# Kernel optimization log

Hardware: AMD Instinct MI355X
Metric: run time of the kernel (lower is better)

## Reference

```python
import jax, jax.numpy as jnp
import numpy as np

VOCAB, EMBED, HIDDEN, LAYERS = 32000, 1024, 1024, 2
BATCH, SEQ = 128, 256


def setup_inputs() -> dict:
    key = jax.random.key(0)
    ks = jax.random.split(key, 6)
    source = jax.random.randint(ks[0], (BATCH, SEQ), 0, VOCAB)
    emb_W = jax.random.normal(ks[1], (VOCAB, EMBED), dtype=jnp.float32) * 0.01
    s = 1.0 / np.sqrt(HIDDEN)
    W_ih = jax.random.uniform(ks[2], (LAYERS, 3 * HIDDEN, EMBED), jnp.float32, -s, s)
    W_hh = jax.random.uniform(ks[3], (LAYERS, 3 * HIDDEN, HIDDEN), jnp.float32, -s, s)
    b_ih = jax.random.uniform(ks[4], (LAYERS, 3 * HIDDEN), jnp.float32, -s, s)
    b_hh = jax.random.uniform(ks[5], (LAYERS, 3 * HIDDEN), jnp.float32, -s, s)
    return {"source": source, "emb_W": emb_W, "W_ih": W_ih, "W_hh": W_hh,
            "b_ih": b_ih, "b_hh": b_hh}


def _gru_layer(xs, h0, Wih, Whh, bih, bhh):
    # xs: [S, B, in], h0: [B, H]; PyTorch GRU cell math.
    def step(h, x):
        gi = x @ Wih.T + bih          # [B, 3H]
        gh = h @ Whh.T + bhh          # [B, 3H]
        ir, iz, inn = jnp.split(gi, 3, axis=-1)
        hr, hz, hn = jnp.split(gh, 3, axis=-1)
        r = jax.nn.sigmoid(ir + hr)
        z = jax.nn.sigmoid(iz + hz)
        n = jnp.tanh(inn + r * hn)
        h_new = (1.0 - z) * n + z * h
        return h_new, h_new
    hT, ys = jax.lax.scan(step, h0, xs)
    return ys, hT


def reference(source, emb_W, W_ih, W_hh, b_ih, b_hh):
    # embedding with transpose=True: [S, B, E]
    embed = emb_W[source.T]
    B = source.shape[0]
    x = embed
    finals = []
    for l in range(W_ih.shape[0]):
        h0 = jnp.zeros((B, W_hh.shape[-1]), dtype=embed.dtype)
        x, hT = _gru_layer(x, h0, W_ih[l], W_hh[l], b_ih[l], b_hh[l])
        finals.append(hT)
    state = jnp.stack(finals, axis=0)  # [L, B, H]
    return x, state
```

## Files before the change

kernel.cpp:

```cpp
#include <hip/hip_runtime.h>
#include <cstdint>
#include <cstddef>

#define SEQ 256
#define BATCH 128
#define HID 1024
#define H3 3072
#define TCH 32
#define NCH (SEQ/TCH)
#define CROWS (TCH*BATCH)

typedef __bf16 bf16x8 __attribute__((ext_vector_type(8)));
typedef float f32x4 __attribute__((ext_vector_type(4)));
typedef unsigned short ushort8 __attribute__((ext_vector_type(8)));
typedef unsigned long long u64x2 __attribute__((ext_vector_type(2)));

static __device__ __forceinline__ unsigned short f2bf(float f){
  unsigned int u = __float_as_uint(f);
  u += 0x7fffu + ((u >> 16) & 1u);
  return (unsigned short)(u >> 16);
}
static __device__ __forceinline__ float sigm(float x){
  return 1.0f / (1.0f + __expf(-x));
}
static __device__ __forceinline__ float tanh_(float x){
  x = fminf(15.0f, fmaxf(-15.0f, x));
  float e = __expf(2.0f * x);
  return (e - 1.0f) / (e + 1.0f);
}


__global__ __launch_bounds__(256) void cvt_bf16(const float* __restrict__ in,
                                                unsigned short* __restrict__ out, int n4){
  int i = blockIdx.x * blockDim.x + threadIdx.x;
  int stride = gridDim.x * blockDim.x;
  for (; i < n4; i += stride){
    float4 v = reinterpret_cast<const float4*>(in)[i];
    ushort4 o = { f2bf(v.x), f2bf(v.y), f2bf(v.z), f2bf(v.w) };
    reinterpret_cast<ushort4*>(out)[i] = o;
  }
}

__global__ __launch_bounds__(256) void embed_gather(const int* __restrict__ src,
                                                    const float* __restrict__ embW,
                                                    unsigned short* __restrict__ x0){
  int bx = blockIdx.x;
  int s = bx >> 7, b = bx & 127;
  int row = src[b * SEQ + s];
  float4 v = reinterpret_cast<const float4*>(embW + (size_t)row * HID)[threadIdx.x];
  ushort4 o = { f2bf(v.x), f2bf(v.y), f2bf(v.z), f2bf(v.w) };
  reinterpret_cast<ushort4*>(x0 + (size_t)bx * HID)[threadIdx.x] = o;
}

__global__ __launch_bounds__(256) void zero_u32(unsigned* __restrict__ p, int n){
  int i = blockIdx.x * blockDim.x + threadIdx.x;
  if (i < n) p[i] = 0u;
}

#define BM 128
#define BN 128
#define BK 32
#define LDT 40

__global__ __launch_bounds__(256) void gemm_xw(
    const unsigned short* __restrict__ A,
    const unsigned short* __restrict__ B,
    float* __restrict__ C)
{
  __shared__ unsigned short As[2][BM][LDT];
  __shared__ unsigned short Bs[2][BN][LDT];
  int tid = threadIdx.x;
  int lane = tid & 63, wid = tid >> 6;
  int fr = lane & 15, kg = lane >> 4;
  int wr = wid >> 1, wc = wid & 1;
  int brow = blockIdx.x * BM;
  int bcol = blockIdx.y * BN;

  int r0 = tid >> 2;
  int r1 = 64 + (tid >> 2);
  int k8 = (tid & 3) * 8;

  const unsigned short* Ab = A + (size_t)brow * HID;
  const unsigned short* Bb = B + (size_t)bcol * HID;

  f32x4 acc[4][4] = {};
  ushort8 a0, a1, b0, b1;

  a0 = *(const ushort8*)(Ab + (size_t)r0 * HID + k8);
  a1 = *(const ushort8*)(Ab + (size_t)r1 * HID + k8);
  b0 = *(const ushort8*)(Bb + (size_t)r0 * HID + k8);
  b1 = *(const ushort8*)(Bb + (size_t)r1 * HID + k8);
  *(ushort8*)&As[0][r0][k8] = a0;
  *(ushort8*)&As[0][r1][k8] = a1;
  *(ushort8*)&Bs[0][r0][k8] = b0;
  *(ushort8*)&Bs[0][r1][k8] = b1;
  __syncthreads();

  for (int kt = 0; kt < HID / BK; ++kt){
    int cur = kt & 1;
    if (kt < HID / BK - 1){
      int ko = (kt + 1) * BK + k8;
      a0 = *(const ushort8*)(Ab + (size_t)r0 * HID + ko);
      a1 = *(const ushort8*)(Ab + (size_t)r1 * HID + ko);
      b0 = *(const ushort8*)(Bb + (size_t)r0 * HID + ko);
      b1 = *(const ushort8*)(Bb + (size_t)r1 * HID + ko);
    }
    bf16x8 af[4], bfr[4];
    #pragma unroll
    for (int m = 0; m < 4; ++m)
      af[m] = *(const bf16x8*)&As[cur][wr*64 + m*16 + fr][kg*8];
    #pragma unroll
    for (int n = 0; n < 4; ++n)
      bfr[n] = *(const bf16x8*)&Bs[cur][wc*64 + n*16 + fr][kg*8];
    #pragma unroll
    for (int m = 0; m < 4; ++m)
      #pragma unroll
      for (int n = 0; n < 4; ++n)
        acc[m][n] = __builtin_amdgcn_mfma_f32_16x16x32_bf16(af[m], bfr[n], acc[m][n], 0,0,0);
    if (kt < HID / BK - 1){
      int nxt = cur ^ 1;
      *(ushort8*)&As[nxt][r0][k8] = a0;
      *(ushort8*)&As[nxt][r1][k8] = a1;
      *(ushort8*)&Bs[nxt][r0][k8] = b0;
      *(ushort8*)&Bs[nxt][r1][k8] = b1;
      __syncthreads();
    }
  }

  #pragma unroll
  for (int m = 0; m < 4; ++m){
    int rowb = brow + wr*64 + m*16 + kg*4;
    #pragma unroll
    for (int n = 0; n < 4; ++n){
      int col = bcol + wc*64 + n*16 + fr;
      *(f32x4*)(C + (size_t)col * CROWS + rowb) = acc[m][n];
    }
  }
}

#define LDW 1032

__global__ __launch_bounds__(256) void gru_persist(
    const unsigned short* __restrict__ Whh,
    const float* __restrict__ bih,
    const float* __restrict__ bhh,
    const float* __restrict__ gi,
    float* __restrict__ ys_out,
    unsigned short* __restrict__ x_next,
    unsigned long long* __restrict__ hbA,
    unsigned long long* __restrict__ hbB,
    float* __restrict__ hf32,
    float* __restrict__ state_out,
    int t0,
    unsigned* __restrict__ cnt)
{
  __shared__ unsigned short Wlds[48 * LDW];
  __shared__ f32x4 red[4][2][3][64];
  __shared__ unsigned short hvt[32][16];

  int tid = threadIdx.x;
  int lane = tid & 63, wid = tid >> 6;
  int ct = blockIdx.x & 63, rg = blockIdx.x >> 6;
  int c0 = ct * 16, rowbase = rg * 32;
  int fr = lane & 15, kg = lane >> 4;

  #pragma unroll
  for (int j = 0; j < 24; ++j){
    int cid = j * 256 + tid;
    int r = cid >> 7, k8 = (cid & 127) * 8;
    int grow = (r >> 4) * HID + c0 + (r & 15);
    *(ushort8*)&Wlds[r * LDW + k8] = *(const ushort8*)(Whh + (size_t)grow * HID + k8);
  }

  int crow = tid >> 3;
  int ccol = (tid << 1) & 15;
  int rt_ = crow >> 4, r16 = crow & 15, kq = r16 >> 2, qq = r16 & 3;
  int l0 = kq * 16 + ccol, l1 = l0 + 1;
  int colc0 = c0 + ccol, colc1 = colc0 + 1;
  int growL = rowbase + crow;

  float br0 = bih[colc0] + bhh[colc0];
  float bz0 = bih[HID + colc0] + bhh[HID + colc0];
  float bi0 = bih[2*HID + colc0];
  float bh0 = bhh[2*HID + colc0];
  float br1 = bih[colc1] + bhh[colc1];
  float bz1 = bih[HID + colc1] + bhh[HID + colc1];
  float bi1 = bih[2*HID + colc1];
  float bh1 = bhh[2*HID + colc1];

  float hprev0 = 0.0f, hprev1 = 0.0f;
  if (t0 > 0){
    hprev0 = hf32[(size_t)growL * HID + colc0];
    hprev1 = hf32[(size_t)growL * HID + colc1];
  }
  __syncthreads();

  for (int s = 0; s < TCH; ++s){
    int t = t0 + s;
    size_t gro = (size_t)s * BATCH + growL;
    float gr0 = gi[(size_t)(0*HID + colc0) * CROWS + gro];
    float gz0 = gi[(size_t)(1*HID + colc0) * CROWS + gro];
    float gn0 = gi[(size_t)(2*HID + colc0) * CROWS + gro];
    float gr1 = gi[(size_t)(0*HID + colc1) * CROWS + gro];
    float gz1 = gi[(size_t)(1*HID + colc1) * CROWS + gro];
    float gn1 = gi[(size_t)(2*HID + colc1) * CROWS + gro];

    if (s > 0){
      if (tid == 0){
        unsigned* p = cnt + rg * TCH + (s - 1);
        int lim = 4000000;
        while (__hip_atomic_load(p, __ATOMIC_RELAXED, __HIP_MEMORY_SCOPE_AGENT) < 64u
               && --lim)
          __builtin_amdgcn_s_sleep(1);
      }
      __syncthreads();
      asm volatile("" ::: "memory");
    }
    const unsigned long long* hin = (t & 1) ? hbB : hbA;
    unsigned long long*       hout = (t & 1) ? hbA : hbB;

    f32x4 acc[2][3] = {};
    if (t > 0){
      const int wk0 = wid << 8;
      bf16x8 a[2][8];
      #pragma unroll
      for (int rt = 0; rt < 2; ++rt){
        size_t rb = (size_t)(rowbase + rt*16 + fr) * HID + wk0 + kg*8;
        #pragma unroll
        for (int j = 0; j < 8; ++j){
          size_t ui = (rb + (size_t)j*32) >> 2;
          unsigned long long u0 = __hip_atomic_load(hin + ui,     __ATOMIC_RELAXED, __HIP_MEMORY_SCOPE_AGENT);
          unsigned long long u1 = __hip_atomic_load(hin + ui + 1, __ATOMIC_RELAXED, __HIP_MEMORY_SCOPE_AGENT);
          u64x2 uu; uu[0] = u0; uu[1] = u1;
          a[rt][j] = __builtin_bit_cast(bf16x8, uu);
        }
      }
      #pragma unroll
      for (int j = 0; j < 8; ++j){
        int bo = wk0 + j*32 + kg*8;
        bf16x8 b0 = *(const bf16x8*)&Wlds[(     fr) * LDW + bo];
        bf16x8 b1 = *(const bf16x8*)&Wlds[(16 + fr) * LDW + bo];
        bf16x8 b2 = *(const bf16x8*)&Wlds[(32 + fr) * LDW + bo];
        acc[0][0] = __builtin_amdgcn_mfma_f32_16x16x32_bf16(a[0][j], b0, acc[0][0], 0,0,0);
        acc[0][1] = __builtin_amdgcn_mfma_f32_16x16x32_bf16(a[0][j], b1, acc[0][1], 0,0,0);
        acc[0][2] = __builtin_amdgcn_mfma_f32_16x16x32_bf16(a[0][j], b2, acc[0][2], 0,0,0);
        acc[1][0] = __builtin_amdgcn_mfma_f32_16x16x32_bf16(a[1][j], b0, acc[1][0], 0,0,0);
        acc[1][1] = __builtin_amdgcn_mfma_f32_16x16x32_bf16(a[1][j], b1, acc[1][1], 0,0,0);
        acc[1][2] = __builtin_amdgcn_mfma_f32_16x16x32_bf16(a[1][j], b2, acc[1][2], 0,0,0);
      }
    }

    #pragma unroll
    for (int rt = 0; rt < 2; ++rt)
      #pragma unroll
      for (int g = 0; g < 3; ++g)
        red[wid][rt][g][lane] = acc[rt][g];
    __syncthreads();

    float v0[3], v1[3];
    #pragma unroll
    for (int g = 0; g < 3; ++g){
      float s0 = 0.f, s1 = 0.f;
      #pragma unroll
      for (int w = 0; w < 4; ++w){
        s0 += red[w][rt_][g][l0][qq];
        s1 += red[w][rt_][g][l1][qq];
      }
      v0[g] = s0; v1[g] = s1;
    }

    float rA = sigm(gr0 + v0[0] + br0);
    float zA = sigm(gz0 + v0[1] + bz0);
    float nA = tanh_(gn0 + bi0 + rA * (v0[2] + bh0));
    float h0 = (1.0f - zA) * nA + zA * hprev0;
    float rB = sigm(gr1 + v1[0] + br1);
    float zB = sigm(gz1 + v1[1] + bz1);
    float nB = tanh_(gn1 + bi1 + rB * (v1[2] + bh1));
    float h1 = (1.0f - zB) * nB + zB * hprev1;
    hprev0 = h0; hprev1 = h1;

    if (ys_out){
      float2 yv = { h0, h1 };
      *(float2*)&ys_out[((size_t)t * BATCH + growL) * HID + colc0] = yv;
    }
    if (x_next){
      ushort2 xv = { f2bf(h0), f2bf(h1) };
      *(ushort2*)&x_next[((size_t)s * BATCH + growL) * HID + colc0] = xv;
    }
    if (t == SEQ-1){
      float2 sv = { h0, h1 };
      *(float2*)&state_out[(size_t)growL * HID + colc0] = sv;
    }
    if (s == TCH-1){
      float2 hv2 = { h0, h1 };
      *(float2*)&hf32[(size_t)growL * HID + colc0] = hv2;
    }

    ushort2 hb2 = { f2bf(h0), f2bf(h1) };
    *(ushort2*)&hvt[crow][ccol] = hb2;
    __syncthreads();

    if (tid < 128){
      int row = tid >> 2, c4 = (tid & 3) * 4;
      unsigned long long u = *(const unsigned long long*)&hvt[row][c4];
      __hip_atomic_store(hout + (((size_t)(rowbase + row) * HID + c0 + c4) >> 2), u,
                         __ATOMIC_RELAXED, __HIP_MEMORY_SCOPE_AGENT);
    }
    __syncthreads();

    if (tid == 0 && s < TCH-1)
      __hip_atomic_fetch_add(cnt + rg * TCH + s, 1u,
                             __ATOMIC_RELAXED, __HIP_MEMORY_SCOPE_AGENT);
  }
}


extern "C" void kernel_launch(void* const* d_in, const int* in_sizes, int n_in,
                              void* d_out, int out_size, void* d_ws, size_t ws_size,
                              hipStream_t stream){
  (void)in_sizes; (void)n_in; (void)out_size; (void)ws_size;
  const int*   src  = (const int*)  d_in[0];
  const float* embW = (const float*)d_in[1];
  const float* Wih  = (const float*)d_in[2];
  const float* Whh  = (const float*)d_in[3];
  const float* bih  = (const float*)d_in[4];
  const float* bhh  = (const float*)d_in[5];
  float* out = (float*)d_out;

  char* ws = (char*)d_ws;
  size_t off = 0;
  auto carve = [&](size_t bytes) -> void* {
    void* p = ws + off;
    off += (bytes + 255) & ~(size_t)255;
    return p;
  };
  const size_t WELEM = (size_t)2 * H3 * HID;
  unsigned short* wihb = (unsigned short*)carve(WELEM * 2);
  unsigned short* whhb = (unsigned short*)carve(WELEM * 2);
  unsigned short* x0   = (unsigned short*)carve((size_t)SEQ*BATCH*HID*2);
  unsigned short* x1   = (unsigned short*)carve((size_t)SEQ*BATCH*HID*2);
  float*          gi   = (float*)         carve((size_t)CROWS*H3*4);
  unsigned long long* hbA = (unsigned long long*)carve((size_t)BATCH*HID*2);
  unsigned long long* hbB = (unsigned long long*)carve((size_t)BATCH*HID*2);
  float*          hf32 = (float*)         carve((size_t)BATCH*HID*4);
  unsigned*       cnt  = (unsigned*)      carve((size_t)16 * 4 * TCH * 4);

  cvt_bf16<<<2048, 256, 0, stream>>>(Wih, wihb, (int)(WELEM/4));
  cvt_bf16<<<2048, 256, 0, stream>>>(Whh, whhb, (int)(WELEM/4));
  embed_gather<<<SEQ*BATCH, 256, 0, stream>>>(src, embW, x0);
  zero_u32<<<8, 256, 0, stream>>>(cnt, 16 * 4 * TCH);

  float* state = out + (size_t)SEQ*BATCH*HID;
  for (int l = 0; l < 2; ++l){
    const float* bihl = bih + l*H3;
    const float* bhhl = bhh + l*H3;
    const unsigned short* wl = wihb + (size_t)l*H3*HID;
    const unsigned short* vl = whhb + (size_t)l*H3*HID;
    for (int cch = 0; cch < NCH; ++cch){
      const unsigned short* Achunk = (l == 0) ? (x0 + (size_t)cch*CROWS*HID)
                                              : (x1 + (size_t)cch*CROWS*HID);
      gemm_xw<<<dim3(CROWS/BM, H3/BN), 256, 0, stream>>>(Achunk, wl, gi);
      int launch_id = l*NCH + cch;
      gru_persist<<<256, 256, 0, stream>>>(
          vl, bihl, bhhl, gi,
          (l == 1) ? out : nullptr,
          (l == 0) ? (x1 + (size_t)cch*CROWS*HID) : nullptr,
          hbA, hbB, hf32,
          state + (size_t)l*BATCH*HID,
          cch*TCH,
          cnt + (size_t)launch_id * 4 * TCH);
    }
  }
}
```

Before: 3.769 ms.

## Restructure GRU recurrence into per-wave row slices with flag-array dependency sync

The persistent GRU kernel now runs 128 threads per block, and each wave owns a 16-row batch slice and computes the full K=1024 reduction itself. This removes the cross-wave LDS reduction and most block-level barriers. The single counter per row group with one polling thread is replaced by per-(step, row slice, column tile) flags, which every lane of a wave polls together. Each wave therefore waits only for the 64 producers of its own 16 rows. The gi inputs for the next step are prefetched and the final hidden state is stored in a lane-native layout. In exchange, each wave does a longer serial MFMA chain, the workspace needs a much larger flag array, and memory ordering now relies on manual waitcnt fences.

```diff
diff --git a/kernel.cpp b/kernel.cpp
--- a/kernel.cpp
+++ b/kernel.cpp
@@ -140,7 +140,7 @@
 
 #define LDW 1032
 
-__global__ __launch_bounds__(256) void gru_persist(
+__global__ __launch_bounds__(128) void gru_persist(
     const unsigned short* __restrict__ Whh,
     const float* __restrict__ bih,
     const float* __restrict__ bhh,
@@ -152,165 +152,135 @@
     float* __restrict__ hf32,
     float* __restrict__ state_out,
     int t0,
-    unsigned* __restrict__ cnt)
+    unsigned* __restrict__ flags)
 {
   __shared__ unsigned short Wlds[48 * LDW];
-  __shared__ f32x4 red[4][2][3][64];
-  __shared__ unsigned short hvt[32][16];
+  __shared__ unsigned short hvt[2][16][16];
 
   int tid = threadIdx.x;
-  int lane = tid & 63, wid = tid >> 6;
-  int ct = blockIdx.x & 63, rg = blockIdx.x >> 6;
-  int c0 = ct * 16, rowbase = rg * 32;
+  int lane = tid & 63, w = tid >> 6;
+  int ct = blockIdx.x & 63, rgp = blockIdx.x >> 6;
+  int c0 = ct * 16;
+  int rs = rgp * 2 + w;
+  int R0 = rs * 16;
   int fr = lane & 15, kg = lane >> 4;
 
   #pragma unroll
-  for (int j = 0; j < 24; ++j){
-    int cid = j * 256 + tid;
+  for (int j = 0; j < 48; ++j){
+    int cid = j * 128 + tid;
     int r = cid >> 7, k8 = (cid & 127) * 8;
     int grow = (r >> 4) * HID + c0 + (r & 15);
     *(ushort8*)&Wlds[r * LDW + k8] = *(const ushort8*)(Whh + (size_t)grow * HID + k8);
   }
 
-  int crow = tid >> 3;
-  int ccol = (tid << 1) & 15;
-  int rt_ = crow >> 4, r16 = crow & 15, kq = r16 >> 2, qq = r16 & 3;
-  int l0 = kq * 16 + ccol, l1 = l0 + 1;
-  int colc0 = c0 + ccol, colc1 = colc0 + 1;
-  int growL = rowbase + crow;
-
-  float br0 = bih[colc0] + bhh[colc0];
-  float bz0 = bih[HID + colc0] + bhh[HID + colc0];
-  float bi0 = bih[2*HID + colc0];
-  float bh0 = bhh[2*HID + colc0];
-  float br1 = bih[colc1] + bhh[colc1];
-  float bz1 = bih[HID + colc1] + bhh[HID + colc1];
-  float bi1 = bih[2*HID + colc1];
-  float bh1 = bhh[2*HID + colc1];
-
-  float hprev0 = 0.0f, hprev1 = 0.0f;
-  if (t0 > 0){
-    hprev0 = hf32[(size_t)growL * HID + colc0];
-    hprev1 = hf32[(size_t)growL * HID + colc1];
-  }
+  int col = c0 + fr;
+  float br_ = bih[col] + bhh[col];
+  float bz_ = bih[HID + col] + bhh[HID + col];
+  float bi_ = bih[2*HID + col];
+  float bh_ = bhh[2*HID + col];
+
+  float* hf_lane = hf32 + (((size_t)blockIdx.x * 2 + w) * 64 + lane) * 4;
+  f32x4 hprev = {0,0,0,0};
+  if (t0 > 0) hprev = *(const f32x4*)hf_lane;
+
+  const float* gib = gi + (size_t)col * CROWS + R0 + kg * 4;
+  const size_t GOFF = (size_t)HID * CROWS;
+
   __syncthreads();
+
+  f32x4 g_r = *(const f32x4*)(gib);
+  f32x4 g_z = *(const f32x4*)(gib + GOFF);
+  f32x4 g_n = *(const f32x4*)(gib + 2*GOFF);
 
   for (int s = 0; s < TCH; ++s){
     int t = t0 + s;
-    size_t gro = (size_t)s * BATCH + growL;
-    float gr0 = gi[(size_t)(0*HID + colc0) * CROWS + gro];
-    float gz0 = gi[(size_t)(1*HID + colc0) * CROWS + gro];
-    float gn0 = gi[(size_t)(2*HID + colc0) * CROWS + gro];
-    float gr1 = gi[(size_t)(0*HID + colc1) * CROWS + gro];
-    float gz1 = gi[(size_t)(1*HID + colc1) * CROWS + gro];
-    float gn1 = gi[(size_t)(2*HID + colc1) * CROWS + gro];
 
     if (s > 0){
-      if (tid == 0){
-        unsigned* p = cnt + rg * TCH + (s - 1);
-        int lim = 4000000;
-        while (__hip_atomic_load(p, __ATOMIC_RELAXED, __HIP_MEMORY_SCOPE_AGENT) < 64u
-               && --lim)
-          __builtin_amdgcn_s_sleep(1);
+      const unsigned* fp = flags + ((s - 1) * 8 + rs) * 64;
+      int lim = 2000000;
+      for (;;){
+        unsigned f = __hip_atomic_load(fp + lane, __ATOMIC_RELAXED, __HIP_MEMORY_SCOPE_AGENT);
+        if (__all(f != 0) || !--lim) break;
+        __builtin_amdgcn_s_sleep(1);
       }
-      __syncthreads();
-      asm volatile("" ::: "memory");
-    }
-    const unsigned long long* hin = (t & 1) ? hbB : hbA;
-    unsigned long long*       hout = (t & 1) ? hbA : hbB;
-
-    f32x4 acc[2][3] = {};
+    }
+
+    f32x4 ngr = {0,0,0,0}, ngz = {0,0,0,0}, ngn = {0,0,0,0};
+    if (s + 1 < TCH){
+      const float* gp = gib + (size_t)(s + 1) * BATCH;
+      ngr = *(const f32x4*)(gp);
+      ngz = *(const f32x4*)(gp + GOFF);
+      ngn = *(const f32x4*)(gp + 2*GOFF);
+    }
+
+    f32x4 accr = {0,0,0,0}, accz = {0,0,0,0}, accn = {0,0,0,0};
     if (t > 0){
-      const int wk0 = wid << 8;
-      bf16x8 a[2][8];
-      #pragma unroll
-      for (int rt = 0; rt < 2; ++rt){
-        size_t rb = (size_t)(rowbase + rt*16 + fr) * HID + wk0 + kg*8;
-        #pragma unroll
-        for (int j = 0; j < 8; ++j){
-          size_t ui = (rb + (size_t)j*32) >> 2;
-          unsigned long long u0 = __hip_atomic_load(hin + ui,     __ATOMIC_RELAXED, __HIP_MEMORY_SCOPE_AGENT);
-          unsigned long long u1 = __hip_atomic_load(hin + ui + 1, __ATOMIC_RELAXED, __HIP_MEMORY_SCOPE_AGENT);
-          u64x2 uu; uu[0] = u0; uu[1] = u1;
-          a[rt][j] = __builtin_bit_cast(bf16x8, uu);
-        }
-      }
-      #pragma unroll
-      for (int j = 0; j < 8; ++j){
-        int bo = wk0 + j*32 + kg*8;
+      const unsigned long long* hin = (t & 1) ? hbB : hbA;
+      const size_t abase = ((size_t)(R0 + fr) * HID + kg * 8) >> 2;
+      #pragma unroll 8
+      for (int ks = 0; ks < 32; ++ks){
+        size_t ai = abase + ks * 8;
+        unsigned long long u0 = __hip_atomic_load(hin + ai,     __ATOMIC_RELAXED, __HIP_MEMORY_SCOPE_AGENT);
+        unsigned long long u1 = __hip_atomic_load(hin + ai + 1, __ATOMIC_RELAXED, __HIP_MEMORY_SCOPE_AGENT);
+        u64x2 uu; uu[0] = u0; uu[1] = u1;
+        bf16x8 a = __builtin_bit_cast(bf16x8, uu);
+        int bo = ks * 32 + kg * 8;
         bf16x8 b0 = *(const bf16x8*)&Wlds[(     fr) * LDW + bo];
         bf16x8 b1 = *(const bf16x8*)&Wlds[(16 + fr) * LDW + bo];
         bf16x8 b2 = *(const bf16x8*)&Wlds[(32 + fr) * LDW + bo];
-        acc[0][0] = __builtin_amdgcn_mfma_f32_16x16x32_bf16(a[0][j], b0, acc[0][0], 0,0,0);
-        acc[0][1] = __builtin_amdgcn_mfma_f32_16x16x32_bf16(a[0][j], b1, acc[0][1], 0,0,0);
-        acc[0][2] = __builtin_amdgcn_mfma_f32_16x16x32_bf16(a[0][j], b2, acc[0][2], 0,0,0);
-        acc[1][0] = __builtin_amdgcn_mfma_f32_16x16x32_bf16(a[1][j], b0, acc[1][0], 0,0,0);
-        acc[1][1] = __builtin_amdgcn_mfma_f32_16x16x32_bf16(a[1][j], b1, acc[1][1], 0,0,0);
-        acc[1][2] = __builtin_amdgcn_mfma_f32_16x16x32_bf16(a[1][j], b2, acc[1][2], 0,0,0);
+        accr = __builtin_amdgcn_mfma_f32_16x16x32_bf16(a, b0, accr, 0,0,0);
+        accz = __builtin_amdgcn_mfma_f32_16x16x32_bf16(a, b1, accz, 0,0,0);
+        accn = __builtin_amdgcn_mfma_f32_16x16x32_bf16(a, b2, accn, 0,0,0);
       }
     }
 
-    #pragma unroll
-    for (int rt = 0; rt < 2; ++rt)
+    f32x4 hnew;
+    #pragma unroll
+    for (int q = 0; q < 4; ++q){
+      float rg_ = sigm(g_r[q] + accr[q] + br_);
+      float zg  = sigm(g_z[q] + accz[q] + bz_);
+      float ng  = tanh_(g_n[q] + bi_ + rg_ * (accn[q] + bh_));
+      hnew[q] = (1.0f - zg) * ng + zg * hprev[q];
+    }
+    hprev = hnew;
+
+    int rowq = R0 + kg * 4;
+    if (ys_out){
       #pragma unroll
-      for (int g = 0; g < 3; ++g)
-        red[wid][rt][g][lane] = acc[rt][g];
-    __syncthreads();
-
-    float v0[3], v1[3];
-    #pragma unroll
-    for (int g = 0; g < 3; ++g){
-      float s0 = 0.f, s1 = 0.f;
+      for (int q = 0; q < 4; ++q)
+        ys_out[((size_t)t * BATCH + rowq + q) * HID + col] = hnew[q];
+    }
+    if (x_next){
       #pragma unroll
-      for (int w = 0; w < 4; ++w){
-        s0 += red[w][rt_][g][l0][qq];
-        s1 += red[w][rt_][g][l1][qq];
-      }
-      v0[g] = s0; v1[g] = s1;
-    }
-
-    float rA = sigm(gr0 + v0[0] + br0);
-    float zA = sigm(gz0 + v0[1] + bz0);
-    float nA = tanh_(gn0 + bi0 + rA * (v0[2] + bh0));
-    float h0 = (1.0f - zA) * nA + zA * hprev0;
-    float rB = sigm(gr1 + v1[0] + br1);
-    float zB = sigm(gz1 + v1[1] + bz1);
-    float nB = tanh_(gn1 + bi1 + rB * (v1[2] + bh1));
-    float h1 = (1.0f - zB) * nB + zB * hprev1;
-    hprev0 = h0; hprev1 = h1;
-
-    if (ys_out){
-      float2 yv = { h0, h1 };
-      *(float2*)&ys_out[((size_t)t * BATCH + growL) * HID + colc0] = yv;
-    }
-    if (x_next){
-      ushort2 xv = { f2bf(h0), f2bf(h1) };
-      *(ushort2*)&x_next[((size_t)s * BATCH + growL) * HID + colc0] = xv;
-    }
-    if (t == SEQ-1){
-      float2 sv = { h0, h1 };
-      *(float2*)&state_out[(size_t)growL * HID + colc0] = sv;
-    }
-    if (s == TCH-1){
-      float2 hv2 = { h0, h1 };
-      *(float2*)&hf32[(size_t)growL * HID + colc0] = hv2;
-    }
-
-    ushort2 hb2 = { f2bf(h0), f2bf(h1) };
-    *(ushort2*)&hvt[crow][ccol] = hb2;
-    __syncthreads();
-
-    if (tid < 128){
-      int row = tid >> 2, c4 = (tid & 3) * 4;
-      unsigned long long u = *(const unsigned long long*)&hvt[row][c4];
-      __hip_atomic_store(hout + (((size_t)(rowbase + row) * HID + c0 + c4) >> 2), u,
+      for (int q = 0; q < 4; ++q)
+        x_next[((size_t)s * BATCH + rowq + q) * HID + col] = f2bf(hnew[q]);
+    }
+    if (t == SEQ - 1){
+      #pragma unroll
+      for (int q = 0; q < 4; ++q)
+        state_out[(size_t)(rowq + q) * HID + col] = hnew[q];
+    }
+    if (s == TCH - 1)
+      *(f32x4*)hf_lane = hprev;
+
+    unsigned long long* hout = (t & 1) ? hbA : hbB;
+    #pragma unroll
+    for (int q = 0; q < 4; ++q)
+      hvt[w][kg*4 + q][fr] = f2bf(hnew[q]);
+    asm volatile("s_waitcnt lgkmcnt(0)" ::: "memory");
+    if (lane < 32){
+      int rr = lane >> 1, cc8 = (lane & 1) * 8;
+      const unsigned long long* hp = (const unsigned long long*)&hvt[w][rr][cc8];
+      size_t ui = ((size_t)(R0 + rr) * HID + c0 + cc8) >> 2;
+      __hip_atomic_store(hout + ui,     hp[0], __ATOMIC_RELAXED, __HIP_MEMORY_SCOPE_AGENT);
+      __hip_atomic_store(hout + ui + 1, hp[1], __ATOMIC_RELAXED, __HIP_MEMORY_SCOPE_AGENT);
+    }
+    asm volatile("s_waitcnt vmcnt(0)" ::: "memory");
+    if (lane == 0)
+      __hip_atomic_store(flags + (s * 8 + rs) * 64 + ct, 1u,
                          __ATOMIC_RELAXED, __HIP_MEMORY_SCOPE_AGENT);
-    }
-    __syncthreads();
-
-    if (tid == 0 && s < TCH-1)
-      __hip_atomic_fetch_add(cnt + rg * TCH + s, 1u,
-                             __ATOMIC_RELAXED, __HIP_MEMORY_SCOPE_AGENT);
+
+    g_r = ngr; g_z = ngz; g_n = ngn;
   }
 }
 
@@ -335,6 +305,7 @@
     return p;
   };
   const size_t WELEM = (size_t)2 * H3 * HID;
+  const int NFLAG = 2 * NCH * TCH * 8 * 64;
   unsigned short* wihb = (unsigned short*)carve(WELEM * 2);
   unsigned short* whhb = (unsigned short*)carve(WELEM * 2);
   unsigned short* x0   = (unsigned short*)carve((size_t)SEQ*BATCH*HID*2);
@@ -342,13 +313,13 @@
   float*          gi   = (float*)         carve((size_t)CROWS*H3*4);
   unsigned long long* hbA = (unsigned long long*)carve((size_t)BATCH*HID*2);
   unsigned long long* hbB = (unsigned long long*)carve((size_t)BATCH*HID*2);
-  float*          hf32 = (float*)         carve((size_t)BATCH*HID*4);
-  unsigned*       cnt  = (unsigned*)      carve((size_t)16 * 4 * TCH * 4);
+  float*          hf32 = (float*)         carve((size_t)512*64*4*4);
+  unsigned*       flags= (unsigned*)      carve((size_t)NFLAG * 4);
 
   cvt_bf16<<<2048, 256, 0, stream>>>(Wih, wihb, (int)(WELEM/4));
   cvt_bf16<<<2048, 256, 0, stream>>>(Whh, whhb, (int)(WELEM/4));
   embed_gather<<<SEQ*BATCH, 256, 0, stream>>>(src, embW, x0);
-  zero_u32<<<8, 256, 0, stream>>>(cnt, 16 * 4 * TCH);
+  zero_u32<<<(NFLAG + 255)/256, 256, 0, stream>>>(flags, NFLAG);
 
   float* state = out + (size_t)SEQ*BATCH*HID;
   for (int l = 0; l < 2; ++l){
@@ -361,14 +332,14 @@
                                               : (x1 + (size_t)cch*CROWS*HID);
       gemm_xw<<<dim3(CROWS/BM, H3/BN), 256, 0, stream>>>(Achunk, wl, gi);
       int launch_id = l*NCH + cch;
-      gru_persist<<<256, 256, 0, stream>>>(
+      gru_persist<<<256, 128, 0, stream>>>(
           vl, bihl, bhhl, gi,
           (l == 1) ? out : nullptr,
           (l == 0) ? (x1 + (size_t)cch*CROWS*HID) : nullptr,
           hbA, hbB, hf32,
           state + (size_t)l*BATCH*HID,
           cch*TCH,
-          cnt + (size_t)launch_id * 4 * TCH);
-    }
-  }
-}
+          flags + (size_t)launch_id * TCH * 8 * 64);
+    }
+  }
+}
```

Result: slower. 7.666 ms (+103.4%).
